# Kernel optimization log

Measured on AMD Instinct MI355X. Metric: run time of the kernel, lower is better.

Reference implementation:

```python
import jax, jax.numpy as jnp
import numpy as np

B, L, D = 4, 512, 768          # batch, seq, d_model
NL, DI, N, K, R = 12, 1536, 16, 4, 48  # layers, d_inner, d_state, d_conv, dt_rank
V, P = 50257, 1024             # vocab, positions
EPS = 1e-5


def setup_inputs() -> dict:
    key = jax.random.key(0)
    ks = jax.random.split(key, 12)
    p = lambda i, shape, s=0.02: jax.random.normal(ks[i], shape, jnp.float32) * s
    return {
        "input_ids": jax.random.randint(ks[0], (B, L), 0, V),
        "wte": p(1, (V, D)),
        "wpe": p(2, (P, D)),
        "ln_g": jnp.ones((NL, D), jnp.float32),
        "ln_b": jnp.zeros((NL, D), jnp.float32),
        "in_W": p(3, (NL, 2 * DI, D)),
        "conv_W": p(4, (NL, DI, K), 0.2),
        "conv_b": jnp.zeros((NL, DI), jnp.float32),
        "xp_W": p(5, (NL, R + 2 * N, DI)),
        "dt_W": p(6, (NL, DI, R), 0.1),
        "dt_b": p(7, (NL, DI), 0.5),
        # Mamba S4D-real init: A = -exp(A_log), A_log = log(1..N)
        "A_log": jnp.tile(jnp.log(jnp.arange(1, N + 1, dtype=jnp.float32)), (NL, DI, 1)),
        "Dres": jnp.ones((NL, DI), jnp.float32),
        "out_W": p(8, (NL, D, DI)),
        "nf_g": jnp.ones((D,), jnp.float32),
        "nf_b": jnp.zeros((D,), jnp.float32),
        "fin_g": jnp.ones((D,), jnp.float32),
        "fin_b": jnp.zeros((D,), jnp.float32),
    }


def layer_norm(x, g, b):
    mu = jnp.mean(x, -1, keepdims=True)
    var = jnp.mean((x - mu) ** 2, -1, keepdims=True)
    return (x - mu) * jax.lax.rsqrt(var + EPS) * g + b


def causal_conv(x, w, b):
    # x: (B, L, DI); depthwise causal conv, kernel K, left pad K-1, truncate to L
    xt = jnp.transpose(x, (0, 2, 1))  # (B, DI, L)
    y = jax.lax.conv_general_dilated(
        xt, w[:, None, :], (1,), [(K - 1, 0)],
        feature_group_count=DI, dimension_numbers=("NCH", "OIH", "NCH"))
    return jnp.transpose(y + b[None, :, None], (0, 2, 1))


def selective_scan(u, delta, A, Bm, Cm):
    # u, delta: (B, L, DI); A: (DI, N); Bm, Cm: (B, L, N)
    def step(h, inp):
        u_t, d_t, b_t, c_t = inp  # (B,DI), (B,DI), (B,N), (B,N)
        dA = jnp.exp(d_t[:, :, None] * A)            # (B, DI, N)
        h = h * dA + (d_t * u_t)[:, :, None] * b_t[:, None, :]
        y = jnp.einsum("bdn,bn->bd", h, c_t)
        return h, y

    h0 = jnp.zeros((u.shape[0], DI, N), u.dtype)
    xs = (jnp.swapaxes(u, 0, 1), jnp.swapaxes(delta, 0, 1),
          jnp.swapaxes(Bm, 0, 1), jnp.swapaxes(Cm, 0, 1))
    _, ys = jax.lax.scan(step, h0, xs)               # ys: (L, B, DI)
    return jnp.swapaxes(ys, 0, 1)


def mamba_mixer(x, inW, cW, cb, xpW, dtW, dtb, a_log, dres, outW):
    xz = jnp.einsum("bld,ed->ble", x, inW)           # (B, L, 2*DI)
    xi, z = jnp.split(xz, 2, axis=-1)
    xi = jax.nn.silu(causal_conv(xi, cW, cb))
    dbl = jnp.einsum("bld,ed->ble", xi, xpW)         # (B, L, R+2N)
    dt, Bm, Cm = dbl[..., :R], dbl[..., R:R + N], dbl[..., R + N:]
    delta = jax.nn.softplus(jnp.einsum("blr,dr->bld", dt, dtW) + dtb)
    A = -jnp.exp(a_log)
    y = selective_scan(xi, delta, A, Bm, Cm) + xi * dres
    y = y * jax.nn.silu(z)
    return jnp.einsum("ble,de->bld", y, outW)


def reference(input_ids, wte, wpe, ln_g, ln_b, in_W, conv_W, conv_b, xp_W,
              dt_W, dt_b, A_log, Dres, out_W, nf_g, nf_b, fin_g, fin_b):
    emb = wte[input_ids] + wpe[: input_ids.shape[1]]  # (B, L, D); dropout=identity (eval)
    hidden, residual = emb, None
    for i in range(NL):
        residual = hidden if residual is None else hidden + residual
        h = layer_norm(residual, ln_g[i], ln_b[i])
        hidden = mamba_mixer(h, in_W[i], conv_W[i], conv_b[i], xp_W[i],
                             dt_W[i], dt_b[i], A_log[i], Dres[i], out_W[i])
    residual = hidden + residual
    out = layer_norm(residual, nf_g, nf_b)   # MixerModel.norm_f
    return layer_norm(out, fin_g, fin_b)     # decoder self.norm
```

## Files before the change

kernel.cpp:

```cpp
#include <hip/hip_runtime.h>

#define BB 4
#define LL 512
#define DD 768
#define NLAYER 12
#define DI 1536
#define NS 16
#define KC 4
#define RR 48
#define MROWS (BB*LL)
#define E2 (2*DI)
#define EPSV 1e-5f
#define CH2 16
#define LC2 (LL/CH2)
#define LOG2E 1.4426950408889634f

typedef __attribute__((ext_vector_type(8))) short bf16x8;
typedef __attribute__((ext_vector_type(4))) float f32x4;

#define GLL16(g, l) __builtin_amdgcn_global_load_lds( \
    (const __attribute__((address_space(1))) void*)(g), \
    (__attribute__((address_space(3))) void*)(l), 16, 0, 0)

__device__ inline float hw_exp2(float x) { return __builtin_amdgcn_exp2f(x); }

__device__ inline ushort f2bf(float f) {
  union { float f; unsigned u; } v; v.f = f;
  unsigned u = v.u;
  unsigned r = (u + 0x7fffu + ((u >> 16) & 1u)) >> 16;
  return (ushort)r;
}
__device__ inline float bf2f(ushort u) {
  union { unsigned u; float f; } v; v.u = ((unsigned)u) << 16; return v.f;
}

__global__ __launch_bounds__(256) void k_embed(const int* __restrict__ ids,
    const float* __restrict__ wte, const float* __restrict__ wpe,
    float* __restrict__ resid) {
  const int nd4 = DD / 4;
  int i = blockIdx.x * 256 + threadIdx.x;
  if (i >= MROWS * nd4) return;
  int m = i / nd4, d4 = i - m * nd4;
  int l = m & (LL - 1);
  int tok = ids[m];
  float4 a = ((const float4*)wte)[(size_t)tok * nd4 + d4];
  float4 b = ((const float4*)wpe)[(size_t)l * nd4 + d4];
  float4 o; o.x = a.x + b.x; o.y = a.y + b.y; o.z = a.z + b.z; o.w = a.w + b.w;
  ((float4*)resid)[i] = o;
}

__device__ inline float block_sum(float v, volatile float* red) {
  #pragma unroll
  for (int o = 32; o > 0; o >>= 1) v += __shfl_down(v, o);
  if ((threadIdx.x & 63) == 0) red[threadIdx.x >> 6] = v;
  __syncthreads();
  float t = red[0] + red[1] + red[2] + red[3];
  __syncthreads();
  return t;
}

__global__ __launch_bounds__(256) void k_ln(const float* __restrict__ h0,
    const float* __restrict__ h1,
    float* __restrict__ resid, const float* __restrict__ g, const float* __restrict__ b,
    ushort* __restrict__ hbf, int addHidden) {
  __shared__ float red[4];
  int m = blockIdx.x, t = threadIdx.x;
  size_t base = (size_t)m * DD;
  float x0 = resid[base + t], x1 = resid[base + t + 256], x2 = resid[base + t + 512];
  if (addHidden) {
    x0 += h0[base + t]       + h1[base + t];
    x1 += h0[base + t + 256] + h1[base + t + 256];
    x2 += h0[base + t + 512] + h1[base + t + 512];
    resid[base + t] = x0; resid[base + t + 256] = x1; resid[base + t + 512] = x2;
  }
  float S  = block_sum(x0 + x1 + x2, red);
  float S2 = block_sum(x0*x0 + x1*x1 + x2*x2, red);
  float mu = S * (1.f / DD);
  float var = S2 * (1.f / DD) - mu * mu;
  float rs = rsqrtf(var + EPSV);
  hbf[base + t]       = f2bf((x0 - mu) * rs * g[t]       + b[t]);
  hbf[base + t + 256] = f2bf((x1 - mu) * rs * g[t + 256] + b[t + 256]);
  hbf[base + t + 512] = f2bf((x2 - mu) * rs * g[t + 512] + b[t + 512]);
}

template<int OM>
__global__ __launch_bounds__(256) void k_gemm128(const ushort* __restrict__ A,
    const ushort* __restrict__ Bw, void* __restrict__ Cv, const float* __restrict__ dtb,
    int N, int K, int kSteps) {
  __shared__ ushort lA[128 * 64];
  __shared__ ushort lB[128 * 64];
  int tid = threadIdx.x;
  int wid = tid >> 6, lane = tid & 63;
  int tm = blockIdx.y * 128, tn = blockIdx.x * 128;
  int kBase = blockIdx.z * kSteps * 64;
  int wr = (wid >> 1) * 64, wc = (wid & 1) * 64;
  int fr = lane & 15, kg = lane >> 4;
  int sR = lane >> 3;
  int sC = ((lane & 7) ^ sR) * 8;
  f32x4 acc[4][4];
  #pragma unroll
  for (int mi = 0; mi < 4; ++mi)
    #pragma unroll
    for (int ni = 0; ni < 4; ++ni)
      acc[mi][ni] = {0.f, 0.f, 0.f, 0.f};

  for (int ks = 0; ks < kSteps; ++ks) {
    int k0 = kBase + ks * 64;
    #pragma unroll
    for (int i = 0; i < 4; ++i) {
      int r0 = wid * 32 + i * 8;
      GLL16(A + (size_t)(tm + r0 + sR) * K + k0 + sC, &lA[r0 * 64]);
      int brow = tn + r0 + sR;
      if (brow > N - 1) brow = N - 1;
      GLL16(Bw + (size_t)brow * K + k0 + sC, &lB[r0 * 64]);
    }
    __syncthreads();
    #pragma unroll
    for (int ks2 = 0; ks2 < 2; ++ks2) {
      bf16x8 af[4], bfr[4];
      #pragma unroll
      for (int mi = 0; mi < 4; ++mi) {
        int row = wr + mi * 16 + fr;
        af[mi] = *(const bf16x8*)&lA[row * 64 + (((ks2 * 4 + kg) ^ (fr & 7)) * 8)];
      }
      #pragma unroll
      for (int ni = 0; ni < 4; ++ni) {
        int row = wc + ni * 16 + fr;
        bfr[ni] = *(const bf16x8*)&lB[row * 64 + (((ks2 * 4 + kg) ^ (fr & 7)) * 8)];
      }
      #pragma unroll
      for (int mi = 0; mi < 4; ++mi)
        #pragma unroll
        for (int ni = 0; ni < 4; ++ni)
          acc[mi][ni] = __builtin_amdgcn_mfma_f32_16x16x32_bf16(af[mi], bfr[ni], acc[mi][ni], 0, 0, 0);
    }
    __syncthreads();
  }
  int crow0 = tm + wr + kg * 4;
  int ccol0 = tn + wc + fr;
  if (OM == 0) {
    float* C = (float*)Cv + (size_t)blockIdx.z * ((size_t)gridDim.y * 128) * N;
    #pragma unroll
    for (int mi = 0; mi < 4; ++mi)
      #pragma unroll
      for (int ni = 0; ni < 4; ++ni) {
        int cc = ccol0 + ni * 16;
        if (cc < N) {
          #pragma unroll
          for (int j = 0; j < 4; ++j)
            C[(size_t)(crow0 + mi * 16 + j) * N + cc] = acc[mi][ni][j];
        }
      }
  } else if (OM == 1) {
    ushort* C = (ushort*)Cv;
    #pragma unroll
    for (int mi = 0; mi < 4; ++mi)
      #pragma unroll
      for (int ni = 0; ni < 4; ++ni) {
        int cc = ccol0 + ni * 16;
        if (cc < N) {
          #pragma unroll
          for (int j = 0; j < 4; ++j)
            C[(size_t)(crow0 + mi * 16 + j) * N + cc] = f2bf(acc[mi][ni][j]);
        }
      }
  } else {
    float* C = (float*)Cv;
    #pragma unroll
    for (int mi = 0; mi < 4; ++mi)
      #pragma unroll
      for (int ni = 0; ni < 4; ++ni) {
        int cc = ccol0 + ni * 16;
        if (cc < N) {
          float bv = dtb[cc];
          #pragma unroll
          for (int j = 0; j < 4; ++j) {
            float x = acc[mi][ni][j] + bv;
            float sp = (x > 20.f) ? x : log1pf(__expf(x));
            C[(size_t)(crow0 + mi * 16 + j) * N + cc] = sp;
          }
        }
      }
  }
}

__global__ __launch_bounds__(256) void k_conv(const ushort* __restrict__ xz,
    const float* __restrict__ cW, const float* __restrict__ cb,
    ushort* __restrict__ xibf, int layer) {
  int i = blockIdx.x * 256 + threadIdx.x;
  if (i >= MROWS * DI) return;
  int c = i % DI;
  int m = i / DI;
  int l = m & (LL - 1);
  const float* w = cW + ((size_t)layer * DI + c) * KC;
  float w0 = w[0], w1 = w[1], w2 = w[2], w3 = w[3];
  float acc = cb[(size_t)layer * DI + c];
  if (l >= 3) {
    size_t base = (size_t)(m - 3) * E2 + c;
    acc += bf2f(xz[base]) * w0 + bf2f(xz[base + E2]) * w1 +
           bf2f(xz[base + 2 * E2]) * w2 + bf2f(xz[base + 3 * E2]) * w3;
  } else {
    #pragma unroll
    for (int k = 0; k < KC; ++k) {
      int ll = l - (KC - 1) + k;
      if (ll >= 0) acc += bf2f(xz[(size_t)(m - (KC - 1) + k) * E2 + c]) *
                          ((k == 0) ? w0 : (k == 1) ? w1 : (k == 2) ? w2 : w3);
    }
  }
  float sg = 1.f / (1.f + __expf(-acc));
  xibf[i] = f2bf(acc * sg);
}

__global__ __launch_bounds__(256) void k_cvt4(const float* __restrict__ s,
    ushort* __restrict__ d, int n4) {
  int i = blockIdx.x * 256 + threadIdx.x;
  if (i >= n4) return;
  float4 v = ((const float4*)s)[i];
  ushort4 o = { f2bf(v.x), f2bf(v.y), f2bf(v.z), f2bf(v.w) };
  ((ushort4*)d)[i] = o;
}

__global__ __launch_bounds__(256) void k_cvt_dtw(const float* __restrict__ s,
    ushort* __restrict__ d, int nRows) {
  int i = blockIdx.x * 256 + threadIdx.x;
  if (i >= nRows * 64) return;
  int r = i >> 6, c = i & 63;
  d[i] = (c < RR) ? f2bf(s[(size_t)r * RR + c]) : (ushort)0;
}

__global__ __launch_bounds__(256) void k_comb_xp(const float* __restrict__ part,
    float* __restrict__ dblb, ushort* __restrict__ dtbf) {
  int i = blockIdx.x * 256 + threadIdx.x;
  if (i >= MROWS * 80) return;
  const int S = MROWS * 80;
  float s = 0.f;
  #pragma unroll
  for (int z = 0; z < 8; ++z) s += part[i + z * S];
  dblb[i] = s;
  int m = i / 80, c = i - m * 80;
  if (c < RR) dtbf[(size_t)m * 64 + c] = f2bf(s);
  else if (c < 64) dtbf[(size_t)m * 64 + c] = 0;
}

__global__ __launch_bounds__(256) void k_scan_f(const float* __restrict__ delta,
    const ushort* __restrict__ ubf, const float* __restrict__ dblb,
    const ushort* __restrict__ xz, const float* __restrict__ A_log,
    const float* __restrict__ Dres, ushort* __restrict__ ybf, int layer) {
  __shared__ float shH[16 * 257];
  __shared__ float shP[16 * 257];
  int tid = threadIdx.x;
  int dloc = tid & 15, chunk = tid >> 4;
  int d = blockIdx.x * 16 + dloc;
  int b = blockIdx.y;
  float an[16];
  {
    const float4* a4 = (const float4*)(A_log + ((size_t)layer * DI + d) * NS);
    #pragma unroll
    for (int q = 0; q < 4; ++q) {
      float4 v = a4[q];
      an[4*q]   = -__expf(v.x) * LOG2E; an[4*q+1] = -__expf(v.y) * LOG2E;
      an[4*q+2] = -__expf(v.z) * LOG2E; an[4*q+3] = -__expf(v.w) * LOG2E;
    }
  }
  int l0 = chunk * LC2;
  size_t rowd0 = ((size_t)b * LL + l0) * DI + d;
  size_t rowb0 = ((size_t)b * LL + l0) * 80 + RR;

  float h[16], pr[16];
  #pragma unroll
  for (int n = 0; n < 16; ++n) { h[n] = 0.f; pr[n] = 1.f; }
  {
    size_t rd = rowd0, rb = rowb0;
    float dl = delta[rd];
    float uv = bf2f(ubf[rd]);
    float4 b0 = *(const float4*)(dblb + rb),     b1 = *(const float4*)(dblb + rb + 4);
    float4 b2 = *(const float4*)(dblb + rb + 8), b3 = *(const float4*)(dblb + rb + 12);
    for (int l = 0; l < LC2; ++l) {
      float dlc = dl, uvc = uv;
      float4 c0 = b0, c1 = b1, c2 = b2, c3 = b3;
      if (l + 1 < LC2) {
        rd += DI; rb += 80;
        dl = delta[rd]; uv = bf2f(ubf[rd]);
        b0 = *(const float4*)(dblb + rb);     b1 = *(const float4*)(dblb + rb + 4);
        b2 = *(const float4*)(dblb + rb + 8); b3 = *(const float4*)(dblb + rb + 12);
      }
      float du = dlc * uvc;
      float Bv[16] = { c0.x, c0.y, c0.z, c0.w, c1.x, c1.y, c1.z, c1.w,
                       c2.x, c2.y, c2.z, c2.w, c3.x, c3.y, c3.z, c3.w };
      #pragma unroll
      for (int n = 0; n < 16; ++n) {
        float a = hw_exp2(dlc * an[n]);
        h[n] = h[n] * a + du * Bv[n];
        pr[n] *= a;
      }
    }
  }
  {
    int base = dloc * 257 + chunk * 16;
    #pragma unroll
    for (int n = 0; n < 16; ++n) { shH[base + n] = h[n]; shP[base + n] = pr[n]; }
  }
  __syncthreads();

  {
    int n2 = tid & 15, dl2 = tid >> 4;
    float hh = 0.f;
    int base = dl2 * 257;
    for (int c = 0; c < CH2; ++c) {
      int idx = base + c * 16 + n2;
      float t = shH[idx], p = shP[idx];
      shH[idx] = hh;
      hh = t + p * hh;
    }
  }
  __syncthreads();

  {
    int base = dloc * 257 + chunk * 16;
    #pragma unroll
    for (int n = 0; n < 16; ++n) h[n] = shH[base + n];
  }
  float dresv = Dres[(size_t)layer * DI + d];
  {
    size_t rd = rowd0, rb = rowb0;
    size_t rz = ((size_t)b * LL + l0) * E2 + DI + d;
    float dl = delta[rd];
    float uv = bf2f(ubf[rd]);
    float4 b0 = *(const float4*)(dblb + rb),      b1 = *(const float4*)(dblb + rb + 4);
    float4 b2 = *(const float4*)(dblb + rb + 8),  b3 = *(const float4*)(dblb + rb + 12);
    float4 e0 = *(const float4*)(dblb + rb + 16), e1 = *(const float4*)(dblb + rb + 20);
    float4 e2 = *(const float4*)(dblb + rb + 24), e3 = *(const float4*)(dblb + rb + 28);
    for (int l = 0; l < LC2; ++l) {
      float dlc = dl, uvc = uv;
      float4 c0 = b0, c1 = b1, c2 = b2, c3 = b3;
      float4 f0 = e0, f1 = e1, f2 = e2, f3 = e3;
      size_t rdc = rd, rzc = rz;
      if (l + 1 < LC2) {
        rd += DI; rb += 80; rz += E2;
        dl = delta[rd]; uv = bf2f(ubf[rd]);
        b0 = *(const float4*)(dblb + rb);      b1 = *(const float4*)(dblb + rb + 4);
        b2 = *(const float4*)(dblb + rb + 8);  b3 = *(const float4*)(dblb + rb + 12);
        e0 = *(const float4*)(dblb + rb + 16); e1 = *(const float4*)(dblb + rb + 20);
        e2 = *(const float4*)(dblb + rb + 24); e3 = *(const float4*)(dblb + rb + 28);
      }
      float du = dlc * uvc;
      float Bv[16] = { c0.x, c0.y, c0.z, c0.w, c1.x, c1.y, c1.z, c1.w,
                       c2.x, c2.y, c2.z, c2.w, c3.x, c3.y, c3.z, c3.w };
      float Cv[16] = { f0.x, f0.y, f0.z, f0.w, f1.x, f1.y, f1.z, f1.w,
                       f2.x, f2.y, f2.z, f2.w, f3.x, f3.y, f3.z, f3.w };
      float y = 0.f;
      #pragma unroll
      for (int n = 0; n < 16; ++n) {
        float a = hw_exp2(dlc * an[n]);
        h[n] = h[n] * a + du * Bv[n];
        y += h[n] * Cv[n];
      }
      float zv = bf2f(xz[rzc]);
      float yt = y + uvc * dresv;
      float sg = 1.f / (1.f + __expf(-zv));
      ybf[rdc] = f2bf(yt * (zv * sg));
    }
  }
}

__global__ __launch_bounds__(256) void k_final(const float* __restrict__ resid,
    const float* __restrict__ h0, const float* __restrict__ h1,
    const float* __restrict__ nfg, const float* __restrict__ nfb,
    const float* __restrict__ fig, const float* __restrict__ fib,
    float* __restrict__ out) {
  __shared__ float red[4];
  int m = blockIdx.x, t = threadIdx.x;
  size_t base = (size_t)m * DD;
  float x0 = resid[base + t]       + h0[base + t]       + h1[base + t];
  float x1 = resid[base + t + 256] + h0[base + t + 256] + h1[base + t + 256];
  float x2 = resid[base + t + 512] + h0[base + t + 512] + h1[base + t + 512];
  float S  = block_sum(x0 + x1 + x2, red);
  float S2 = block_sum(x0*x0 + x1*x1 + x2*x2, red);
  float mu = S * (1.f / DD);
  float var = S2 * (1.f / DD) - mu * mu;
  float rs = rsqrtf(var + EPSV);
  float t0 = (x0 - mu) * rs * nfg[t]       + nfb[t];
  float t1 = (x1 - mu) * rs * nfg[t + 256] + nfb[t + 256];
  float t2 = (x2 - mu) * rs * nfg[t + 512] + nfb[t + 512];
  S  = block_sum(t0 + t1 + t2, red);
  S2 = block_sum(t0*t0 + t1*t1 + t2*t2, red);
  mu = S * (1.f / DD);
  var = S2 * (1.f / DD) - mu * mu;
  rs = rsqrtf(var + EPSV);
  out[base + t]       = (t0 - mu) * rs * fig[t]       + fib[t];
  out[base + t + 256] = (t1 - mu) * rs * fig[t + 256] + fib[t + 256];
  out[base + t + 512] = (t2 - mu) * rs * fig[t + 512] + fib[t + 512];
}

extern "C" void kernel_launch(void* const* d_in, const int* in_sizes, int n_in,
                              void* d_out, int out_size, void* d_ws, size_t ws_size,
                              hipStream_t stream) {
  const int*   ids    = (const int*)  d_in[0];
  const float* wte    = (const float*)d_in[1];
  const float* wpe    = (const float*)d_in[2];
  const float* ln_g   = (const float*)d_in[3];
  const float* ln_b   = (const float*)d_in[4];
  const float* in_W   = (const float*)d_in[5];
  const float* conv_W = (const float*)d_in[6];
  const float* conv_b = (const float*)d_in[7];
  const float* xp_W   = (const float*)d_in[8];
  const float* dt_W   = (const float*)d_in[9];
  const float* dt_b   = (const float*)d_in[10];
  const float* A_log  = (const float*)d_in[11];
  const float* Dres   = (const float*)d_in[12];
  const float* out_W  = (const float*)d_in[13];
  const float* nf_g   = (const float*)d_in[14];
  const float* nf_b   = (const float*)d_in[15];
  const float* fin_g  = (const float*)d_in[16];
  const float* fin_b  = (const float*)d_in[17];

  char* p = (char*)d_ws;
  auto take = [&](size_t bytes) {
    char* r = p; p += (bytes + 255) & ~(size_t)255; return r;
  };
  float*  resid  = (float*) take((size_t)MROWS * DD * 4);
  float*  hidP   = (float*) take((size_t)2 * MROWS * DD * 4);
  ushort* h_bf   = (ushort*)take((size_t)MROWS * DD * 2);
  ushort* xz     = (ushort*)take((size_t)MROWS * E2 * 2);
  ushort* xibf   = (ushort*)take((size_t)MROWS * DI * 2);
  float*  xpPart = (float*) take((size_t)8 * MROWS * 80 * 4);
  float*  dblb   = (float*) take((size_t)MROWS * 80 * 4);
  ushort* dtbf   = (ushort*)take((size_t)MROWS * 64 * 2);
  float*  delta  = (float*) take((size_t)MROWS * DI * 4);
  ushort* ybf    = (ushort*)take((size_t)MROWS * DI * 2);
  ushort* wInBf  = (ushort*)take((size_t)NLAYER * E2 * DD * 2);
  ushort* wXpBf  = (ushort*)take((size_t)NLAYER * 80 * DI * 2);
  ushort* wDtBf  = (ushort*)take((size_t)NLAYER * DI * 64 * 2);
  ushort* wOutBf = (ushort*)take((size_t)NLAYER * DD * DI * 2);

  k_cvt4<<<(NLAYER * E2 * DD / 4 + 255) / 256, 256, 0, stream>>>(in_W, wInBf, NLAYER * E2 * DD / 4);
  k_cvt4<<<(NLAYER * 80 * DI / 4 + 255) / 256, 256, 0, stream>>>(xp_W, wXpBf, NLAYER * 80 * DI / 4);
  k_cvt_dtw<<<(NLAYER * DI * 64 + 255) / 256, 256, 0, stream>>>(dt_W, wDtBf, NLAYER * DI);
  k_cvt4<<<(NLAYER * DD * DI / 4 + 255) / 256, 256, 0, stream>>>(out_W, wOutBf, NLAYER * DD * DI / 4);

  k_embed<<<(MROWS * (DD / 4) + 255) / 256, 256, 0, stream>>>(ids, wte, wpe, resid);

  for (int i = 0; i < NLAYER; ++i) {
    k_ln<<<MROWS, 256, 0, stream>>>(hidP, hidP + (size_t)MROWS * DD, resid,
                                    ln_g + (size_t)i * DD, ln_b + (size_t)i * DD,
                                    h_bf, i > 0 ? 1 : 0);

    { dim3 g(E2 / 128, MROWS / 128, 1);
      k_gemm128<1><<<g, 256, 0, stream>>>(h_bf, wInBf + (size_t)i * E2 * DD,
                                          (void*)xz, nullptr, E2, DD, DD / 64); }

    k_conv<<<((MROWS * DI) + 255) / 256, 256, 0, stream>>>(xz, conv_W, conv_b, xibf, i);

    { dim3 g(1, MROWS / 128, 8);
      k_gemm128<0><<<g, 256, 0, stream>>>(xibf, wXpBf + (size_t)i * 80 * DI,
                                          (void*)xpPart, nullptr, 80, DI, DI / 64 / 8); }

    k_comb_xp<<<(MROWS * 80 + 255) / 256, 256, 0, stream>>>(xpPart, dblb, dtbf);

    { dim3 g(DI / 128, MROWS / 128, 1);
      k_gemm128<2><<<g, 256, 0, stream>>>(dtbf, wDtBf + (size_t)i * DI * 64,
                                          (void*)delta, dt_b + (size_t)i * DI, DI, 64, 1); }

    { dim3 g(DI / 16, BB);
      k_scan_f<<<g, 256, 0, stream>>>(delta, xibf, dblb, xz, A_log, Dres, ybf, i); }

    { dim3 g(DD / 128, MROWS / 128, 2);
      k_gemm128<0><<<g, 256, 0, stream>>>(ybf, wOutBf + (size_t)i * DD * DI,
                                          (void*)hidP, nullptr, DD, DI, DI / 64 / 2); }
  }

  k_final<<<MROWS, 256, 0, stream>>>(resid, hidP, hidP + (size_t)MROWS * DD,
                                     nf_g, nf_b, fin_g, fin_b, (float*)d_out);
}
```

Before: 1.596 ms.

## Fuse causal conv+SiLU into x_proj GEMM A-tile load and merge weight conversions

Adds a k_xpconv kernel that computes the depthwise causal conv and SiLU straight from xz while filling the GEMM's LDS A tile. It writes the xi result to global for the scan and runs the x_proj MFMA in the same kernel, with split-K raised from 8 to 12. Conv weights are transposed once so eight channels can be loaded as vectors. The four weight-conversion launches become two, which removes a per-layer kernel launch and one read of xibf. In exchange, each block does redundant conv halo reads, and the combine step sums more split-K partials.

```diff
diff --git a/kernel.cpp b/kernel.cpp
--- a/kernel.cpp
+++ b/kernel.cpp
@@ -14,6 +14,7 @@
 #define CH2 16
 #define LC2 (LL/CH2)
 #define LOG2E 1.4426950408889634f
+#define XPZ 12
 
 typedef __attribute__((ext_vector_type(8))) short bf16x8;
 typedef __attribute__((ext_vector_type(4))) float f32x4;
@@ -32,6 +33,58 @@
 }
 __device__ inline float bf2f(ushort u) {
   union { unsigned u; float f; } v; v.u = ((unsigned)u) << 16; return v.f;
+}
+
+__device__ inline float block_sum(float v, volatile float* red) {
+  #pragma unroll
+  for (int o = 32; o > 0; o >>= 1) v += __shfl_down(v, o);
+  if ((threadIdx.x & 63) == 0) red[threadIdx.x >> 6] = v;
+  __syncthreads();
+  float t = red[0] + red[1] + red[2] + red[3];
+  __syncthreads();
+  return t;
+}
+
+__global__ __launch_bounds__(256) void k_cvtA(const float* __restrict__ inW,
+    const float* __restrict__ outW, ushort* __restrict__ wIn,
+    ushort* __restrict__ wOut) {
+  int i = blockIdx.x * 256 + threadIdx.x;
+  const int nIn = NLAYER * E2 * DD / 4;
+  const int nOut = NLAYER * DD * DI / 4;
+  if (i < nIn) {
+    float4 v = ((const float4*)inW)[i];
+    ushort4 o = { f2bf(v.x), f2bf(v.y), f2bf(v.z), f2bf(v.w) };
+    ((ushort4*)wIn)[i] = o;
+  } else if (i < nIn + nOut) {
+    int j = i - nIn;
+    float4 v = ((const float4*)outW)[j];
+    ushort4 o = { f2bf(v.x), f2bf(v.y), f2bf(v.z), f2bf(v.w) };
+    ((ushort4*)wOut)[j] = o;
+  }
+}
+
+__global__ __launch_bounds__(256) void k_cvtB(const float* __restrict__ xpW,
+    const float* __restrict__ dtW, const float* __restrict__ convW,
+    ushort* __restrict__ wXp, ushort* __restrict__ wDt, float* __restrict__ convWt) {
+  int i = blockIdx.x * 256 + threadIdx.x;
+  const int n0 = NLAYER * 80 * DI / 4;
+  const int n1 = NLAYER * DI * 64;
+  const int n2 = NLAYER * DI * 4;
+  if (i < n0) {
+    float4 v = ((const float4*)xpW)[i];
+    ushort4 o = { f2bf(v.x), f2bf(v.y), f2bf(v.z), f2bf(v.w) };
+    ((ushort4*)wXp)[i] = o;
+  } else if (i < n0 + n1) {
+    int j = i - n0;
+    int r = j >> 6, c = j & 63;
+    wDt[j] = (c < RR) ? f2bf(dtW[(size_t)r * RR + c]) : (ushort)0;
+  } else if (i < n0 + n1 + n2) {
+    int j = i - n0 - n1;
+    int l = j / (DI * 4);
+    int rem = j - l * (DI * 4);
+    int d = rem >> 2, k = rem & 3;
+    convWt[(size_t)l * 4 * DI + k * DI + d] = convW[(size_t)l * DI * 4 + d * 4 + k];
+  }
 }
 
 __global__ __launch_bounds__(256) void k_embed(const int* __restrict__ ids,
@@ -47,16 +100,6 @@
   float4 b = ((const float4*)wpe)[(size_t)l * nd4 + d4];
   float4 o; o.x = a.x + b.x; o.y = a.y + b.y; o.z = a.z + b.z; o.w = a.w + b.w;
   ((float4*)resid)[i] = o;
-}
-
-__device__ inline float block_sum(float v, volatile float* red) {
-  #pragma unroll
-  for (int o = 32; o > 0; o >>= 1) v += __shfl_down(v, o);
-  if ((threadIdx.x & 63) == 0) red[threadIdx.x >> 6] = v;
-  __syncthreads();
-  float t = red[0] + red[1] + red[2] + red[3];
-  __syncthreads();
-  return t;
 }
 
 __global__ __launch_bounds__(256) void k_ln(const float* __restrict__ h0,
@@ -116,18 +159,14 @@
     }
     __syncthreads();
     #pragma unroll
-    for (int ks2 = 0; ks2 < 2; ++ks2) {
+    for (int k2 = 0; k2 < 2; ++k2) {
       bf16x8 af[4], bfr[4];
       #pragma unroll
-      for (int mi = 0; mi < 4; ++mi) {
-        int row = wr + mi * 16 + fr;
-        af[mi] = *(const bf16x8*)&lA[row * 64 + (((ks2 * 4 + kg) ^ (fr & 7)) * 8)];
-      }
-      #pragma unroll
-      for (int ni = 0; ni < 4; ++ni) {
-        int row = wc + ni * 16 + fr;
-        bfr[ni] = *(const bf16x8*)&lB[row * 64 + (((ks2 * 4 + kg) ^ (fr & 7)) * 8)];
-      }
+      for (int mi = 0; mi < 4; ++mi)
+        af[mi] = *(const bf16x8*)&lA[(wr + mi * 16 + fr) * 64 + (((k2 * 4 + kg) ^ (fr & 7)) * 8)];
+      #pragma unroll
+      for (int ni = 0; ni < 4; ++ni)
+        bfr[ni] = *(const bf16x8*)&lB[(wc + ni * 16 + fr) * 64 + (((k2 * 4 + kg) ^ (fr & 7)) * 8)];
       #pragma unroll
       for (int mi = 0; mi < 4; ++mi)
         #pragma unroll
@@ -184,48 +223,100 @@
   }
 }
 
-__global__ __launch_bounds__(256) void k_conv(const ushort* __restrict__ xz,
-    const float* __restrict__ cW, const float* __restrict__ cb,
-    ushort* __restrict__ xibf, int layer) {
-  int i = blockIdx.x * 256 + threadIdx.x;
-  if (i >= MROWS * DI) return;
-  int c = i % DI;
-  int m = i / DI;
-  int l = m & (LL - 1);
-  const float* w = cW + ((size_t)layer * DI + c) * KC;
-  float w0 = w[0], w1 = w[1], w2 = w[2], w3 = w[3];
-  float acc = cb[(size_t)layer * DI + c];
-  if (l >= 3) {
-    size_t base = (size_t)(m - 3) * E2 + c;
-    acc += bf2f(xz[base]) * w0 + bf2f(xz[base + E2]) * w1 +
-           bf2f(xz[base + 2 * E2]) * w2 + bf2f(xz[base + 3 * E2]) * w3;
-  } else {
-    #pragma unroll
-    for (int k = 0; k < KC; ++k) {
-      int ll = l - (KC - 1) + k;
-      if (ll >= 0) acc += bf2f(xz[(size_t)(m - (KC - 1) + k) * E2 + c]) *
-                          ((k == 0) ? w0 : (k == 1) ? w1 : (k == 2) ? w2 : w3);
-    }
-  }
-  float sg = 1.f / (1.f + __expf(-acc));
-  xibf[i] = f2bf(acc * sg);
-}
-
-__global__ __launch_bounds__(256) void k_cvt4(const float* __restrict__ s,
-    ushort* __restrict__ d, int n4) {
-  int i = blockIdx.x * 256 + threadIdx.x;
-  if (i >= n4) return;
-  float4 v = ((const float4*)s)[i];
-  ushort4 o = { f2bf(v.x), f2bf(v.y), f2bf(v.z), f2bf(v.w) };
-  ((ushort4*)d)[i] = o;
-}
-
-__global__ __launch_bounds__(256) void k_cvt_dtw(const float* __restrict__ s,
-    ushort* __restrict__ d, int nRows) {
-  int i = blockIdx.x * 256 + threadIdx.x;
-  if (i >= nRows * 64) return;
-  int r = i >> 6, c = i & 63;
-  d[i] = (c < RR) ? f2bf(s[(size_t)r * RR + c]) : (ushort)0;
+__global__ __launch_bounds__(256) void k_xpconv(const ushort* __restrict__ xz,
+    const ushort* __restrict__ wXpL, const float* __restrict__ cwt,
+    const float* __restrict__ cbl, ushort* __restrict__ xibf,
+    float* __restrict__ xpPart) {
+  __shared__ ushort lA[128 * 64];
+  __shared__ ushort lB[128 * 64];
+  int tid = threadIdx.x;
+  int wid = tid >> 6, lane = tid & 63;
+  int tm2 = blockIdx.y * 128;
+  int kBase = blockIdx.z * 128;
+  int wr = (wid >> 1) * 64, wc = (wid & 1) * 64;
+  int fr = lane & 15, kg = lane >> 4;
+  int sR = lane >> 3, sC = ((lane & 7) ^ sR) * 8;
+  f32x4 acc[4][4];
+  #pragma unroll
+  for (int mi = 0; mi < 4; ++mi)
+    #pragma unroll
+    for (int ni = 0; ni < 4; ++ni)
+      acc[mi][ni] = {0.f, 0.f, 0.f, 0.f};
+  for (int ks = 0; ks < 2; ++ks) {
+    int k0 = kBase + ks * 64;
+    #pragma unroll
+    for (int i2 = 0; i2 < 4; ++i2) {
+      int r0 = wid * 32 + i2 * 8;
+      int brow = r0 + sR;
+      if (brow > 79) brow = 79;
+      GLL16(wXpL + (size_t)brow * DI + k0 + sC, &lB[r0 * 64]);
+    }
+    #pragma unroll
+    for (int c2 = 0; c2 < 4; ++c2) {
+      int chunk = tid + c2 * 256;
+      int row = chunk >> 3, cc8 = chunk & 7;
+      int m = tm2 + row, l = m & (LL - 1);
+      int gc = k0 + cc8 * 8;
+      float a8[8];
+      {
+        float4 a = *(const float4*)&cbl[gc];
+        float4 b = *(const float4*)&cbl[gc + 4];
+        a8[0] = a.x; a8[1] = a.y; a8[2] = a.z; a8[3] = a.w;
+        a8[4] = b.x; a8[5] = b.y; a8[6] = b.z; a8[7] = b.w;
+      }
+      #pragma unroll
+      for (int t = 0; t < 4; ++t) {
+        if (l - 3 + t >= 0) {
+          float4 a = *(const float4*)&cwt[t * DI + gc];
+          float4 b = *(const float4*)&cwt[t * DI + gc + 4];
+          bf16x8 v = *(const bf16x8*)&xz[(size_t)(m - 3 + t) * E2 + gc];
+          a8[0] += bf2f((ushort)v[0]) * a.x; a8[1] += bf2f((ushort)v[1]) * a.y;
+          a8[2] += bf2f((ushort)v[2]) * a.z; a8[3] += bf2f((ushort)v[3]) * a.w;
+          a8[4] += bf2f((ushort)v[4]) * b.x; a8[5] += bf2f((ushort)v[5]) * b.y;
+          a8[6] += bf2f((ushort)v[6]) * b.z; a8[7] += bf2f((ushort)v[7]) * b.w;
+        }
+      }
+      bf16x8 vo;
+      #pragma unroll
+      for (int j = 0; j < 8; ++j) {
+        float sg = 1.f / (1.f + __expf(-a8[j]));
+        vo[j] = (short)f2bf(a8[j] * sg);
+      }
+      *(bf16x8*)&lA[row * 64 + ((cc8 ^ (row & 7)) * 8)] = vo;
+      *(bf16x8*)&xibf[(size_t)m * DI + gc] = vo;
+    }
+    __syncthreads();
+    #pragma unroll
+    for (int k2 = 0; k2 < 2; ++k2) {
+      bf16x8 af[4], bf4[4];
+      #pragma unroll
+      for (int mi = 0; mi < 4; ++mi)
+        af[mi] = *(const bf16x8*)&lA[(wr + mi * 16 + fr) * 64 + (((k2 * 4 + kg) ^ (fr & 7)) * 8)];
+      #pragma unroll
+      for (int ni = 0; ni < 4; ++ni)
+        bf4[ni] = *(const bf16x8*)&lB[(wc + ni * 16 + fr) * 64 + (((k2 * 4 + kg) ^ (fr & 7)) * 8)];
+      #pragma unroll
+      for (int mi = 0; mi < 4; ++mi)
+        #pragma unroll
+        for (int ni = 0; ni < 4; ++ni)
+          acc[mi][ni] = __builtin_amdgcn_mfma_f32_16x16x32_bf16(af[mi], bf4[ni], acc[mi][ni], 0, 0, 0);
+    }
+    __syncthreads();
+  }
+  int crow0 = tm2 + wr + kg * 4;
+  int ccol0 = wc + fr;
+  float* Cf = xpPart + (size_t)blockIdx.z * MROWS * 80;
+  #pragma unroll
+  for (int mi = 0; mi < 4; ++mi)
+    #pragma unroll
+    for (int ni = 0; ni < 4; ++ni) {
+      int cc = ccol0 + ni * 16;
+      if (cc < 80) {
+        #pragma unroll
+        for (int j = 0; j < 4; ++j)
+          Cf[(size_t)(crow0 + mi * 16 + j) * 80 + cc] = acc[mi][ni][j];
+      }
+    }
 }
 
 __global__ __launch_bounds__(256) void k_comb_xp(const float* __restrict__ part,
@@ -235,7 +326,7 @@
   const int S = MROWS * 80;
   float s = 0.f;
   #pragma unroll
-  for (int z = 0; z < 8; ++z) s += part[i + z * S];
+  for (int z = 0; z < XPZ; ++z) s += part[i + z * S];
   dblb[i] = s;
   int m = i / 80, c = i - m * 80;
   if (c < RR) dtbf[(size_t)m * 64 + c] = f2bf(s);
@@ -301,7 +392,6 @@
     for (int n = 0; n < 16; ++n) { shH[base + n] = h[n]; shP[base + n] = pr[n]; }
   }
   __syncthreads();
-
   {
     int n2 = tid & 15, dl2 = tid >> 4;
     float hh = 0.f;
@@ -314,7 +404,6 @@
     }
   }
   __syncthreads();
-
   {
     int base = dloc * 257 + chunk * 16;
     #pragma unroll
@@ -423,7 +512,7 @@
   ushort* h_bf   = (ushort*)take((size_t)MROWS * DD * 2);
   ushort* xz     = (ushort*)take((size_t)MROWS * E2 * 2);
   ushort* xibf   = (ushort*)take((size_t)MROWS * DI * 2);
-  float*  xpPart = (float*) take((size_t)8 * MROWS * 80 * 4);
+  float*  xpPart = (float*) take((size_t)XPZ * MROWS * 80 * 4);
   float*  dblb   = (float*) take((size_t)MROWS * 80 * 4);
   ushort* dtbf   = (ushort*)take((size_t)MROWS * 64 * 2);
   float*  delta  = (float*) take((size_t)MROWS * DI * 4);
@@ -432,12 +521,17 @@
   ushort* wXpBf  = (ushort*)take((size_t)NLAYER * 80 * DI * 2);
   ushort* wDtBf  = (ushort*)take((size_t)NLAYER * DI * 64 * 2);
   ushort* wOutBf = (ushort*)take((size_t)NLAYER * DD * DI * 2);
-
-  k_cvt4<<<(NLAYER * E2 * DD / 4 + 255) / 256, 256, 0, stream>>>(in_W, wInBf, NLAYER * E2 * DD / 4);
-  k_cvt4<<<(NLAYER * 80 * DI / 4 + 255) / 256, 256, 0, stream>>>(xp_W, wXpBf, NLAYER * 80 * DI / 4);
-  k_cvt_dtw<<<(NLAYER * DI * 64 + 255) / 256, 256, 0, stream>>>(dt_W, wDtBf, NLAYER * DI);
-  k_cvt4<<<(NLAYER * DD * DI / 4 + 255) / 256, 256, 0, stream>>>(out_W, wOutBf, NLAYER * DD * DI / 4);
-
+  float*  convWt = (float*) take((size_t)NLAYER * 4 * DI * 4);
+
+  {
+    int total = NLAYER * E2 * DD / 4 + NLAYER * DD * DI / 4;
+    k_cvtA<<<(total + 255) / 256, 256, 0, stream>>>(in_W, out_W, wInBf, wOutBf);
+  }
+  {
+    int total = NLAYER * 80 * DI / 4 + NLAYER * DI * 64 + NLAYER * DI * 4;
+    k_cvtB<<<(total + 255) / 256, 256, 0, stream>>>(xp_W, dt_W, conv_W,
+                                                    wXpBf, wDtBf, convWt);
+  }
   k_embed<<<(MROWS * (DD / 4) + 255) / 256, 256, 0, stream>>>(ids, wte, wpe, resid);
 
   for (int i = 0; i < NLAYER; ++i) {
@@ -449,11 +543,10 @@
       k_gemm128<1><<<g, 256, 0, stream>>>(h_bf, wInBf + (size_t)i * E2 * DD,
                                           (void*)xz, nullptr, E2, DD, DD / 64); }
 
-    k_conv<<<((MROWS * DI) + 255) / 256, 256, 0, stream>>>(xz, conv_W, conv_b, xibf, i);
-
-    { dim3 g(1, MROWS / 128, 8);
-      k_gemm128<0><<<g, 256, 0, stream>>>(xibf, wXpBf + (size_t)i * 80 * DI,
-                                          (void*)xpPart, nullptr, 80, DI, DI / 64 / 8); }
+    { dim3 g(1, MROWS / 128, XPZ);
+      k_xpconv<<<g, 256, 0, stream>>>(xz, wXpBf + (size_t)i * 80 * DI,
+                                      convWt + (size_t)i * 4 * DI,
+                                      conv_b + (size_t)i * DI, xibf, xpPart); }
 
     k_comb_xp<<<(MROWS * 80 + 255) / 256, 256, 0, stream>>>(xpPart, dblb, dtbf);
 
```

Result: no change. 1.595 ms (-0.0%).
